# Performance work log

Measured on AMD Instinct MI355X. Metric: run time of the kernel, lower is better.

Reference implementation:

```python
import jax, jax.numpy as jnp
import numpy as np

H = 2048        # hidden_size
NH = 16         # num query heads
NKV = 4         # num kv heads
HD = H // NH    # head_dim = 128
G = NH // NKV   # kv groups = 4
EPS = 1e-12


def setup_inputs() -> dict:
    key = jax.random.key(0)
    ks = jax.random.split(key, 20)
    B, S = 2, 2048
    s = 1.0 / np.sqrt(H)
    inp = {
        "hidden_states": jax.random.normal(ks[0], (B, S, H), jnp.float32),
        "source_states": jax.random.normal(ks[1], (B, S, H), jnp.float32),
        # weights stored [in, out] so y = x @ W + b
        "Wq": jax.random.normal(ks[2], (H, NH * HD), jnp.float32) * s,
        "bq": jnp.zeros((NH * HD,), jnp.float32),
        "Wk": jax.random.normal(ks[3], (H, NKV * HD), jnp.float32) * s,
        "bk": jnp.zeros((NKV * HD,), jnp.float32),
        "Wv": jax.random.normal(ks[4], (H, NKV * HD), jnp.float32) * s,
        "bv": jnp.zeros((NKV * HD,), jnp.float32),
        "Wd": jax.random.normal(ks[5], (H, H), jnp.float32) * s,
        "bd": jnp.zeros((H,), jnp.float32),
        "W1": jax.random.normal(ks[6], (H, H), jnp.float32) * s,
        "b1": jnp.zeros((H,), jnp.float32),
        "W2": jax.random.normal(ks[7], (H, H), jnp.float32) * s,
        "b2": jnp.zeros((H,), jnp.float32),
        "gamma": jnp.ones((H,), jnp.float32),
        "beta": jnp.zeros((H,), jnp.float32),
    }
    return inp


def _layernorm(x, gamma, beta):
    mu = jnp.mean(x, axis=-1, keepdims=True)
    var = jnp.mean(jnp.square(x - mu), axis=-1, keepdims=True)
    return (x - mu) * jax.lax.rsqrt(var + EPS) * gamma + beta


def reference(hidden_states, source_states, Wq, bq, Wk, bk, Wv, bv, Wd, bd,
              W1, b1, W2, b2, gamma, beta):
    B, Sq, _ = hidden_states.shape
    Ss = source_states.shape[1]
    # FFN-gate on source: Pl1 = relu(lin1(src)); P = lin2(Pl1) + Pl1
    Pl1 = jax.nn.relu(source_states @ W1 + b1)
    P = (Pl1 @ W2 + b2) + Pl1
    # projections; K/V grouped into NKV heads, Q into NH = NKV*G heads
    K = (P @ Wk + bk).reshape(B, Ss, NKV, HD).transpose(0, 2, 1, 3)        # b k s d
    V = (P @ Wv + bv).reshape(B, Ss, NKV, HD).transpose(0, 2, 1, 3)        # b k s d
    Q = (hidden_states @ Wq + bq).reshape(B, Sq, NKV, G, HD)
    Q = Q.transpose(0, 2, 3, 1, 4)                                          # b k g q d
    scores = jnp.einsum('bkgqd,bksd->bkgqs', Q, K) / np.sqrt(HD)
    probs = jax.nn.softmax(scores, axis=-1)
    ctx = jnp.einsum('bkgqs,bksd->bkgqd', probs, V)                         # b k g q d
    ctx = ctx.transpose(0, 3, 1, 2, 4).reshape(B, Sq, NH * HD)              # b q h*d
    out = ctx @ Wd + bd
    return _layernorm(out + hidden_states, gamma, beta)
```

## Files before the change

kernel.cpp:

```cpp
#include <hip/hip_runtime.h>
#include <hip/hip_bf16.h>

typedef __bf16 bf16;
typedef __bf16 bf16x4 __attribute__((ext_vector_type(4)));
typedef __bf16 bf16x8 __attribute__((ext_vector_type(8)));
typedef float  f32x4  __attribute__((ext_vector_type(4)));

#define H_   2048
#define S_   2048
#define B_   2
#define NH_  16
#define NKV_ 4
#define HD_  128
#define KVS  1024

#define QSCALE 0.12751743f

__device__ __forceinline__ f32x4 mfma16(bf16x8 a, bf16x8 b, f32x4 c) {
  return __builtin_amdgcn_mfma_f32_16x16x32_bf16(a, b, c, 0, 0, 0);
}

typedef __attribute__((address_space(3))) unsigned int lds_u32_t;
typedef const __attribute__((address_space(1))) unsigned int glb_u32_t;
__device__ __forceinline__ void glds16(const bf16* g, bf16* l) {
  __builtin_amdgcn_global_load_lds((glb_u32_t*)g, (lds_u32_t*)l, 16, 0, 0);
}

__global__ __launch_bounds__(256)
void prep(const float* __restrict__ Wq, const float* __restrict__ W1,
          const float* __restrict__ W2, const float* __restrict__ Wd,
          const float* __restrict__ Wk, const float* __restrict__ Wv,
          const float* __restrict__ hidden, const float* __restrict__ source,
          bf16* __restrict__ Wqt, bf16* __restrict__ W1t,
          bf16* __restrict__ W2t, bf16* __restrict__ Wdt,
          bf16* __restrict__ Wkt, bf16* __restrict__ Wvt,
          bf16* __restrict__ hb,  bf16* __restrict__ sb)
{
  __shared__ bf16 t[32][33];
  int idx = blockIdx.x;
  if (idx < 16384) {
    const float* in = (idx < 8192) ? hidden : source;
    bf16*       out = (idx < 8192) ? hb : sb;
    const int i = idx & 8191;
    const size_t off = ((size_t)i * 256 + threadIdx.x) * 4;
    const float4 v = *(const float4*)(in + off);
    bf16x4 o = { (bf16)v.x, (bf16)v.y, (bf16)v.z, (bf16)v.w };
    *(bf16x4*)(out + off) = o;
    return;
  }
  idx -= 16384;
  const float* in; bf16* out; int N;
  if      (idx < 4096)  { in = Wq; out = Wqt; N = 2048; }
  else if (idx < 8192)  { in = W1; out = W1t; N = 2048; idx -= 4096; }
  else if (idx < 12288) { in = W2; out = W2t; N = 2048; idx -= 8192; }
  else if (idx < 16384) { in = Wd; out = Wdt; N = 2048; idx -= 12288; }
  else if (idx < 17408) { in = Wk; out = Wkt; N = 512;  idx -= 16384; }
  else                  { in = Wv; out = Wvt; N = 512;  idx -= 17408; }
  const int K = 2048;
  const int tx = threadIdx.x & 31, ty = threadIdx.x >> 5;
  const int k0 = (idx & 63) * 32, n0 = (idx >> 6) * 32;
  #pragma unroll
  for (int i = 0; i < 4; i++)
    t[ty + i*8][tx] = (bf16)in[(size_t)(k0 + ty + i*8) * N + n0 + tx];
  __syncthreads();
  #pragma unroll
  for (int i = 0; i < 4; i++)
    out[(size_t)(n0 + ty + i*8) * K + k0 + tx] = t[tx][ty + i*8];
}

__global__ __launch_bounds__(256)
void transpose_v(const bf16* __restrict__ KVin, bf16* __restrict__ Vt)
{
  __shared__ bf16 t[32][33];
  const int tx = threadIdx.x & 31, ty = threadIdx.x >> 5;
  const int s0 = blockIdx.x * 32, d0 = blockIdx.y * 32;
  const int bk = blockIdx.z;
  const int b = bk >> 2, kv = bk & 3;
  const bf16* src = KVin + (size_t)b * S_ * KVS + 512 + kv * HD_;
  #pragma unroll
  for (int i = 0; i < 4; i++)
    t[ty + i*8][tx] = src[(size_t)(s0 + ty + i*8) * KVS + d0 + tx];
  __syncthreads();
  bf16* dst = Vt + (size_t)bk * HD_ * S_;
  #pragma unroll
  for (int i = 0; i < 4; i++)
    dst[(size_t)(d0 + ty + i*8) * S_ + s0 + tx] = t[tx][ty + i*8];
}

__device__ __forceinline__
void gemm_body(const bf16* __restrict__ A, const bf16* __restrict__ Wt,
               const float* __restrict__ bias, const float* __restrict__ bias2,
               int nsplit, const bf16* __restrict__ resid,
               bf16* __restrict__ outB, int N, int K, int relu, float oscale,
               int m0, int n0, bf16* As, bf16* Bs)
{
  const int tid  = threadIdx.x;
  const int lane = tid & 63;
  const int w    = tid >> 6;
  const int wm = w & 1, wn = w >> 1;
  const int quad = lane >> 4, l16 = lane & 15;
  const int g_r = lane >> 2;
  const int g_c = (lane & 3) * 8;

  const f32x4 fz = {0.f, 0.f, 0.f, 0.f};
  f32x4 acc[4][4];
  #pragma unroll
  for (int i = 0; i < 4; i++)
    #pragma unroll
    for (int j = 0; j < 4; j++) acc[i][j] = fz;

  auto stage = [&](int nb, int k0) {
    #pragma unroll
    for (int i = 0; i < 2; i++) {
      const int rb = (w*2 + i) * 16;
      glds16(A  + (size_t)(m0 + rb + g_r) * K + k0 + g_c, As + nb*4096 + rb*32 + lane*8);
      glds16(Wt + (size_t)(n0 + rb + g_r) * K + k0 + g_c, Bs + nb*4096 + rb*32 + lane*8);
    }
  };

  stage(0, 0);
  const int NK = K >> 5;
  for (int it = 0; it < NK; it++) {
    const int bf = it & 1;
    __syncthreads();
    if (it + 1 < NK) stage(bf ^ 1, (it + 1) << 5);
    bf16x8 af[4], bfr[4];
    #pragma unroll
    for (int i = 0; i < 4; i++)
      af[i]  = *(const bf16x8*)(As + bf*4096 + (wm*64 + i*16 + l16)*32 + quad*8);
    #pragma unroll
    for (int j = 0; j < 4; j++)
      bfr[j] = *(const bf16x8*)(Bs + bf*4096 + (wn*64 + j*16 + l16)*32 + quad*8);
    #pragma unroll
    for (int i = 0; i < 4; i++)
      #pragma unroll
      for (int j = 0; j < 4; j++)
        acc[i][j] = mfma16(af[i], bfr[j], acc[i][j]);
  }

  #pragma unroll
  for (int i = 0; i < 4; i++) {
    const int row = m0 + wm*64 + i*16 + quad*4;
    #pragma unroll
    for (int j = 0; j < 4; j++) {
      const int col = n0 + wn*64 + j*16 + l16;
      const float bi = (col < nsplit) ? bias[col] : bias2[col - nsplit];
      #pragma unroll
      for (int r = 0; r < 4; r++) {
        float v = acc[i][j][r] + bi;
        if (relu) v = fmaxf(v, 0.f);
        v *= oscale;
        size_t idx = (size_t)(row + r) * N + col;
        if (resid) v += (float)resid[idx];
        outB[idx] = (bf16)v;
      }
    }
  }
}

__global__ __launch_bounds__(256)
void gemm_one(const bf16* __restrict__ A, const bf16* __restrict__ Wt,
              const float* __restrict__ bias, const float* __restrict__ bias2,
              int nsplit, const bf16* __restrict__ resid,
              bf16* __restrict__ outB, int N, int K, int relu, float oscale)
{
  __shared__ __align__(16) bf16 As[2*128*32];
  __shared__ __align__(16) bf16 Bs[2*128*32];
  gemm_body(A, Wt, bias, bias2, nsplit, resid, outB, N, K, relu, oscale,
            blockIdx.y*128, blockIdx.x*128, As, Bs);
}

__global__ __launch_bounds__(256)
void gemm_dual(const bf16* __restrict__ A0, const bf16* __restrict__ W0,
               const float* __restrict__ b0, bf16* __restrict__ o0,
               int relu0, float s0,
               const bf16* __restrict__ A1, const bf16* __restrict__ W1,
               const float* __restrict__ b1, bf16* __restrict__ o1,
               int relu1, float s1, int N, int K)
{
  __shared__ __align__(16) bf16 As[2*128*32];
  __shared__ __align__(16) bf16 Bs[2*128*32];
  if (blockIdx.z == 0)
    gemm_body(A0, W0, b0, b0, 1<<30, nullptr, o0, N, K, relu0, s0,
              blockIdx.y*128, blockIdx.x*128, As, Bs);
  else
    gemm_body(A1, W1, b1, b1, 1<<30, nullptr, o1, N, K, relu1, s1,
              blockIdx.y*128, blockIdx.x*128, As, Bs);
}

__global__ __launch_bounds__(256)
void attn_partial(const bf16* __restrict__ Q, const bf16* __restrict__ KV,
                  const bf16* __restrict__ Vt, bf16* __restrict__ OpBase,
                  float* __restrict__ LsBase)
{
  __shared__ __align__(16) bf16 Ks[2][4][32][32];
  __shared__ __align__(16) bf16 Vs[2][8][16][32];
  __shared__ __align__(16) bf16 Ps[4][32][40];
  const int tid = threadIdx.x;
  const int lane = tid & 63, w = tid >> 6;
  const int quad = lane >> 4, l16 = lane & 15;
  const int qt = blockIdx.x, h = blockIdx.y;
  const int b = blockIdx.z >> 1, sh = blockIdx.z & 1;
  const int kv = h >> 2;
  const int qbase = qt * 128 + w * 32;
  const int s_begin = sh * (S_/2);

  bf16*  Op = OpBase + (size_t)sh * 8388608;
  float* Lp = LsBase + (size_t)sh * (B_*NH_*S_);

  const bf16* Qp = Q  + ((size_t)b * S_ + qbase) * H_ + h * HD_;
  const bf16* Kp = KV + (size_t)b * S_ * KVS + kv * HD_;
  const bf16* Vp = Vt + (size_t)(b * NKV_ + kv) * HD_ * S_;

  const int g_r = lane >> 2;
  const int g_c = (lane & 3) * 8;

  const f32x4 fz = {0.f, 0.f, 0.f, 0.f};

  bf16x8 qf[2][4];
  #pragma unroll
  for (int i = 0; i < 2; i++)
    #pragma unroll
    for (int kt = 0; kt < 4; kt++)
      qf[i][kt] = *(const bf16x8*)(Qp + (size_t)(i*16 + l16) * H_ + kt*32 + quad*8);

  f32x4 o[2][8];
  #pragma unroll
  for (int i = 0; i < 2; i++)
    #pragma unroll
    for (int n = 0; n < 8; n++) o[i][n] = fz;
  float lsum[2][4];
  #pragma unroll
  for (int i = 0; i < 2; i++)
    #pragma unroll
    for (int r = 0; r < 4; r++) lsum[i][r] = 0.f;

  const int rd_sw = ((l16 >> 2) & 3) * 8;

  {
    const int s0 = s_begin;
    glds16(Kp + (size_t)(s0 +      g_r) * KVS + w*32 + g_c, &Ks[0][w][0][0]   + lane*8);
    glds16(Kp + (size_t)(s0 + 16 + g_r) * KVS + w*32 + g_c, &Ks[0][w][16][0]  + lane*8);
    glds16(Vp + (size_t)(w*16     + g_r) * S_ + s0 + g_c,   &Vs[0][w][0][0]   + lane*8);
    glds16(Vp + (size_t)((4+w)*16 + g_r) * S_ + s0 + g_c,   &Vs[0][4+w][0][0] + lane*8);
  }

  const int NIT = (S_/2) / 32;
  for (int it = 0; it < NIT; it++) {
    const int bf = it & 1;
    __syncthreads();
    if (it + 1 < NIT) {
      const int s0 = s_begin + (it + 1) * 32;
      const int nb = bf ^ 1;
      glds16(Kp + (size_t)(s0 +      g_r) * KVS + w*32 + g_c, &Ks[nb][w][0][0]   + lane*8);
      glds16(Kp + (size_t)(s0 + 16 + g_r) * KVS + w*32 + g_c, &Ks[nb][w][16][0]  + lane*8);
      glds16(Vp + (size_t)(w*16     + g_r) * S_ + s0 + g_c,   &Vs[nb][w][0][0]   + lane*8);
      glds16(Vp + (size_t)((4+w)*16 + g_r) * S_ + s0 + g_c,   &Vs[nb][4+w][0][0] + lane*8);
    }

    f32x4 sa[2][2];
    sa[0][0] = fz; sa[0][1] = fz; sa[1][0] = fz; sa[1][1] = fz;
    #pragma unroll
    for (int kt = 0; kt < 4; kt++) {
      bf16x8 kf0 = *(const bf16x8*)(&Ks[bf][kt][l16][quad*8]);
      bf16x8 kf1 = *(const bf16x8*)(&Ks[bf][kt][16 + l16][quad*8]);
      #pragma unroll
      for (int i = 0; i < 2; i++) {
        sa[i][0] = mfma16(qf[i][kt], kf0, sa[i][0]);
        sa[i][1] = mfma16(qf[i][kt], kf1, sa[i][1]);
      }
    }
    #pragma unroll
    for (int i = 0; i < 2; i++)
      #pragma unroll
      for (int nt = 0; nt < 2; nt++)
        #pragma unroll
        for (int r = 0; r < 4; r++) {
          float p = exp2f(sa[i][nt][r]);
          lsum[i][r] += p;
          Ps[w][i*16 + quad*4 + r][(nt*16 + l16) ^ (quad*8)] = (bf16)p;
        }
    bf16x8 pf[2];
    #pragma unroll
    for (int i = 0; i < 2; i++)
      pf[i] = *(const bf16x8*)(&Ps[w][i*16 + l16][(quad*8) ^ rd_sw]);
    #pragma unroll
    for (int nt = 0; nt < 8; nt++) {
      bf16x8 vf = *(const bf16x8*)(&Vs[bf][nt][l16][quad*8]);
      #pragma unroll
      for (int i = 0; i < 2; i++)
        o[i][nt] = mfma16(pf[i], vf, o[i][nt]);
    }
  }

  #pragma unroll
  for (int i = 0; i < 2; i++)
    #pragma unroll
    for (int r = 0; r < 4; r++) {
      float s = lsum[i][r];
      s += __shfl_xor(s, 1);
      s += __shfl_xor(s, 2);
      s += __shfl_xor(s, 4);
      s += __shfl_xor(s, 8);
      lsum[i][r] = s;
    }

  bf16* op = Op + ((size_t)b * S_ + qbase) * H_ + h * HD_;
  #pragma unroll
  for (int i = 0; i < 2; i++)
    #pragma unroll
    for (int nt = 0; nt < 8; nt++)
      #pragma unroll
      for (int r = 0; r < 4; r++)
        op[(size_t)(i*16 + quad*4 + r) * H_ + nt*16 + l16] = (bf16)o[i][nt][r];
  if (l16 == 0) {
    float* lp = Lp + (size_t)(b * NH_ + h) * S_ + qbase;
    #pragma unroll
    for (int i = 0; i < 2; i++)
      #pragma unroll
      for (int r = 0; r < 4; r++)
        lp[i*16 + quad*4 + r] = lsum[i][r];
  }
}

__global__ __launch_bounds__(256)
void attn_combine(const bf16* __restrict__ O0, const bf16* __restrict__ O1,
                  const float* __restrict__ L0, const float* __restrict__ L1,
                  bf16* __restrict__ ctx)
{
  const int row = blockIdx.x;
  const int b = row >> 11, s = row & 2047;
  const int tid = threadIdx.x;
  const int h = tid >> 4;
  const size_t idx = (size_t)row * H_ + tid * 8;
  const size_t li  = (size_t)(b * NH_ + h) * S_ + s;
  const float rinv = 1.f / (L0[li] + L1[li]);
  bf16x8 a = *(const bf16x8*)(O0 + idx);
  bf16x8 c = *(const bf16x8*)(O1 + idx);
  bf16x8 o;
  #pragma unroll
  for (int k = 0; k < 8; k++)
    o[k] = (bf16)(((float)a[k] + (float)c[k]) * rinv);
  *(bf16x8*)(ctx + idx) = o;
}

__global__ __launch_bounds__(256)
void ln_fused(const bf16* __restrict__ a, const float* __restrict__ hidden,
              const float* __restrict__ gamma, const float* __restrict__ beta,
              float* __restrict__ out)
{
  __shared__ float red[8];
  const int row = blockIdx.x;
  const bf16*  pa = a      + (size_t)row * H_;
  const float* pb = hidden + (size_t)row * H_;
  float x[8]; float s = 0.f, s2 = 0.f;
  #pragma unroll
  for (int j = 0; j < 8; j++) {
    int c = threadIdx.x + j*256;
    float v = (float)pa[c] + pb[c];
    x[j] = v; s += v; s2 += v*v;
  }
  #pragma unroll
  for (int off = 1; off < 64; off <<= 1) {
    s  += __shfl_xor(s,  off);
    s2 += __shfl_xor(s2, off);
  }
  const int wv = threadIdx.x >> 6;
  if ((threadIdx.x & 63) == 0) { red[wv] = s; red[4 + wv] = s2; }
  __syncthreads();
  s  = red[0] + red[1] + red[2] + red[3];
  s2 = red[4] + red[5] + red[6] + red[7];
  const float mu   = s * (1.0f / H_);
  const float var  = s2 * (1.0f / H_) - mu * mu;
  const float rstd = rsqrtf(var + 1e-12f);
  float* po = out + (size_t)row * H_;
  #pragma unroll
  for (int j = 0; j < 8; j++) {
    int c = threadIdx.x + j*256;
    po[c] = ((x[j] - mu) * rstd) * gamma[c] + beta[c];
  }
}

extern "C" void kernel_launch(void* const* d_in, const int* in_sizes, int n_in,
                              void* d_out, int out_size, void* d_ws, size_t ws_size,
                              hipStream_t stream)
{
  (void)in_sizes; (void)n_in; (void)out_size; (void)ws_size;
  const float* hidden = (const float*)d_in[0];
  const float* source = (const float*)d_in[1];
  const float* Wq = (const float*)d_in[2];
  const float* bq = (const float*)d_in[3];
  const float* Wk = (const float*)d_in[4];
  const float* bk = (const float*)d_in[5];
  const float* Wv = (const float*)d_in[6];
  const float* bv = (const float*)d_in[7];
  const float* Wd = (const float*)d_in[8];
  const float* bd = (const float*)d_in[9];
  const float* W1 = (const float*)d_in[10];
  const float* b1 = (const float*)d_in[11];
  const float* W2 = (const float*)d_in[12];
  const float* b2 = (const float*)d_in[13];
  const float* gamma = (const float*)d_in[14];
  const float* beta  = (const float*)d_in[15];

  char* ws = (char*)d_ws;
  const size_t M = 1048576;
  bf16*  rHB = (bf16*)(ws + 0*M);
  bf16*  rSB = (bf16*)(ws + 16*M);
  bf16*  Qb  = (bf16*)(ws + 32*M);
  bf16*  Wqt = (bf16*)(ws + 48*M);
  bf16*  W2t = (bf16*)(ws + 56*M);
  bf16*  W1t = (bf16*)(ws + 64*M);
  bf16*  Wdt = (bf16*)(ws + 72*M);
  bf16*  Wkt = (bf16*)(ws + 80*M);
  bf16*  Wvt = (bf16*)(ws + 82*M);
  bf16*  Pl1 = (bf16*)(ws + 84*M);
  bf16*  KVb = (bf16*)(ws + 84*M);
  bf16*  Vtb = (bf16*)(ws + 92*M);
  float* Ls  = (float*)(ws + 48*M);
  bf16*  Pb  = rHB;
  bf16*  O0  = rHB;
  bf16*  O1  = rSB;
  bf16*  ctx = (bf16*)(ws + 56*M);
  bf16*  oFb = Qb;

  prep<<<34816, 256, 0, stream>>>(Wq, W1, W2, Wd, Wk, Wv, hidden, source,
                                  Wqt, W1t, W2t, Wdt, Wkt, Wvt, rHB, rSB);
  gemm_dual<<<dim3(16,32,2), 256, 0, stream>>>(
      rHB, Wqt, bq, Qb,  0, QSCALE,
      rSB, W1t, b1, Pl1, 1, 1.0f, 2048, 2048);
  gemm_one<<<dim3(16,32), 256, 0, stream>>>(Pl1, W2t, b2, b2, 1<<30, Pl1,
                                            Pb, 2048, 2048, 0, 1.0f);
  gemm_one<<<dim3(8,32), 256, 0, stream>>>(Pb, Wkt, bk, bv, 512, nullptr,
                                           KVb, 1024, 2048, 0, 1.0f);
  transpose_v<<<dim3(64,4,8), 256, 0, stream>>>(KVb, Vtb);
  attn_partial<<<dim3(16,16,4), 256, 0, stream>>>(Qb, KVb, Vtb, O0, Ls);
  attn_combine<<<4096, 256, 0, stream>>>(O0, O1, Ls, Ls + B_*NH_*S_, ctx);
  gemm_one<<<dim3(16,32), 256, 0, stream>>>(ctx, Wdt, bd, bd, 1<<30, nullptr,
                                            oFb, 2048, 2048, 0, 1.0f);
  ln_fused<<<4096, 256, 0, stream>>>(oFb, hidden, gamma, beta, (float*)d_out);
}
```

Before: 600.9 us.

## Keep attention probabilities in registers via transposed QK MFMA and lane shuffles

The QK^T MFMA operands are swapped so each lane holds scores for one query row. The probabilities are then packed to bf16 and redistributed with lane shuffles into the PV A-operand layout, replacing the LDS round trip through the Ps buffer. K/V staging now uses a flat fragment-major LDS layout so fragment reads are contiguous per lane. The change also adds s_setprio around the MFMA blocks and launch_bounds(256,4) to raise occupancy, at the cost of extra shuffle instructions and register pressure.

```diff
diff --git a/kernel.cpp b/kernel.cpp
--- a/kernel.cpp
+++ b/kernel.cpp
@@ -2,9 +2,11 @@
 #include <hip/hip_bf16.h>
 
 typedef __bf16 bf16;
+typedef __bf16 bf16x2 __attribute__((ext_vector_type(2)));
 typedef __bf16 bf16x4 __attribute__((ext_vector_type(4)));
 typedef __bf16 bf16x8 __attribute__((ext_vector_type(8)));
 typedef float  f32x4  __attribute__((ext_vector_type(4)));
+typedef unsigned int u32x4 __attribute__((ext_vector_type(4)));
 
 #define H_   2048
 #define S_   2048
@@ -24,6 +26,11 @@
 typedef const __attribute__((address_space(1))) unsigned int glb_u32_t;
 __device__ __forceinline__ void glds16(const bf16* g, bf16* l) {
   __builtin_amdgcn_global_load_lds((glb_u32_t*)g, (lds_u32_t*)l, 16, 0, 0);
+}
+
+__device__ __forceinline__ unsigned pk2(float a, float b) {
+  bf16x2 v = { (bf16)a, (bf16)b };
+  return __builtin_bit_cast(unsigned, v);
 }
 
 __global__ __launch_bounds__(256)
@@ -188,14 +195,13 @@
               blockIdx.y*128, blockIdx.x*128, As, Bs);
 }
 
-__global__ __launch_bounds__(256)
+__global__ __launch_bounds__(256, 4)
 void attn_partial(const bf16* __restrict__ Q, const bf16* __restrict__ KV,
                   const bf16* __restrict__ Vt, bf16* __restrict__ OpBase,
                   float* __restrict__ LsBase)
 {
-  __shared__ __align__(16) bf16 Ks[2][4][32][32];
-  __shared__ __align__(16) bf16 Vs[2][8][16][32];
-  __shared__ __align__(16) bf16 Ps[4][32][40];
+  __shared__ __align__(16) bf16 Ks[2*4096];
+  __shared__ __align__(16) bf16 Vs[2*4096];
   const int tid = threadIdx.x;
   const int lane = tid & 63, w = tid >> 6;
   const int quad = lane >> 4, l16 = lane & 15;
@@ -212,8 +218,8 @@
   const bf16* Kp = KV + (size_t)b * S_ * KVS + kv * HD_;
   const bf16* Vp = Vt + (size_t)(b * NKV_ + kv) * HD_ * S_;
 
-  const int g_r = lane >> 2;
-  const int g_c = (lane & 3) * 8;
+  const int fr = lane & 15;
+  const int fc = (lane >> 4) * 8;
 
   const f32x4 fz = {0.f, 0.f, 0.f, 0.f};
 
@@ -229,81 +235,80 @@
   for (int i = 0; i < 2; i++)
     #pragma unroll
     for (int n = 0; n < 8; n++) o[i][n] = fz;
-  float lsum[2][4];
-  #pragma unroll
-  for (int i = 0; i < 2; i++)
-    #pragma unroll
-    for (int r = 0; r < 4; r++) lsum[i][r] = 0.f;
-
-  const int rd_sw = ((l16 >> 2) & 3) * 8;
-
-  {
-    const int s0 = s_begin;
-    glds16(Kp + (size_t)(s0 +      g_r) * KVS + w*32 + g_c, &Ks[0][w][0][0]   + lane*8);
-    glds16(Kp + (size_t)(s0 + 16 + g_r) * KVS + w*32 + g_c, &Ks[0][w][16][0]  + lane*8);
-    glds16(Vp + (size_t)(w*16     + g_r) * S_ + s0 + g_c,   &Vs[0][w][0][0]   + lane*8);
-    glds16(Vp + (size_t)((4+w)*16 + g_r) * S_ + s0 + g_c,   &Vs[0][4+w][0][0] + lane*8);
-  }
+  float lsum[2] = {0.f, 0.f};
+
+  auto stageKV = [&](int nb, int s0) {
+    bf16* Kb = Ks + nb*4096;
+    bf16* Vb = Vs + nb*4096;
+    glds16(Kp + (size_t)(s0 +      fr) * KVS + w*32 + fc, Kb + (w*2+0)*512 + lane*8);
+    glds16(Kp + (size_t)(s0 + 16 + fr) * KVS + w*32 + fc, Kb + (w*2+1)*512 + lane*8);
+    glds16(Vp + (size_t)(w*16     + fr) * S_ + s0 + fc,   Vb + w*512       + lane*8);
+    glds16(Vp + (size_t)((4+w)*16 + fr) * S_ + s0 + fc,   Vb + (4+w)*512   + lane*8);
+  };
+
+  stageKV(0, s_begin);
 
   const int NIT = (S_/2) / 32;
   for (int it = 0; it < NIT; it++) {
     const int bf = it & 1;
     __syncthreads();
-    if (it + 1 < NIT) {
-      const int s0 = s_begin + (it + 1) * 32;
-      const int nb = bf ^ 1;
-      glds16(Kp + (size_t)(s0 +      g_r) * KVS + w*32 + g_c, &Ks[nb][w][0][0]   + lane*8);
-      glds16(Kp + (size_t)(s0 + 16 + g_r) * KVS + w*32 + g_c, &Ks[nb][w][16][0]  + lane*8);
-      glds16(Vp + (size_t)(w*16     + g_r) * S_ + s0 + g_c,   &Vs[nb][w][0][0]   + lane*8);
-      glds16(Vp + (size_t)((4+w)*16 + g_r) * S_ + s0 + g_c,   &Vs[nb][4+w][0][0] + lane*8);
-    }
-
+    if (it + 1 < NIT) stageKV(bf ^ 1, s_begin + (it + 1) * 32);
+
+    const bf16* Kb = Ks + bf*4096;
     f32x4 sa[2][2];
     sa[0][0] = fz; sa[0][1] = fz; sa[1][0] = fz; sa[1][1] = fz;
+    __builtin_amdgcn_s_setprio(1);
     #pragma unroll
     for (int kt = 0; kt < 4; kt++) {
-      bf16x8 kf0 = *(const bf16x8*)(&Ks[bf][kt][l16][quad*8]);
-      bf16x8 kf1 = *(const bf16x8*)(&Ks[bf][kt][16 + l16][quad*8]);
+      bf16x8 kf0 = *(const bf16x8*)(Kb + (kt*2+0)*512 + lane*8);
+      bf16x8 kf1 = *(const bf16x8*)(Kb + (kt*2+1)*512 + lane*8);
       #pragma unroll
       for (int i = 0; i < 2; i++) {
-        sa[i][0] = mfma16(qf[i][kt], kf0, sa[i][0]);
-        sa[i][1] = mfma16(qf[i][kt], kf1, sa[i][1]);
+        sa[i][0] = mfma16(kf0, qf[i][kt], sa[i][0]);
+        sa[i][1] = mfma16(kf1, qf[i][kt], sa[i][1]);
       }
     }
-    #pragma unroll
-    for (int i = 0; i < 2; i++)
+    __builtin_amdgcn_s_setprio(0);
+
+    bf16x8 pf[2];
+    #pragma unroll
+    for (int i = 0; i < 2; i++) {
+      float p[2][4];
       #pragma unroll
       for (int nt = 0; nt < 2; nt++)
         #pragma unroll
         for (int r = 0; r < 4; r++) {
-          float p = exp2f(sa[i][nt][r]);
-          lsum[i][r] += p;
-          Ps[w][i*16 + quad*4 + r][(nt*16 + l16) ^ (quad*8)] = (bf16)p;
+          p[nt][r] = exp2f(sa[i][nt][r]);
+          lsum[i] += p[nt][r];
         }
-    bf16x8 pf[2];
-    #pragma unroll
-    for (int i = 0; i < 2; i++)
-      pf[i] = *(const bf16x8*)(&Ps[w][i*16 + l16][(quad*8) ^ rd_sw]);
+      unsigned Apk = pk2(p[0][0], p[0][1]);
+      unsigned Bpk = pk2(p[0][2], p[0][3]);
+      unsigned Cpk = pk2(p[1][0], p[1][1]);
+      unsigned Dpk = pk2(p[1][2], p[1][3]);
+      const int srcL = l16 + ((quad & 1) << 5);
+      const bool hi = (quad >= 2);
+      const unsigned a0 = __shfl(Apk, srcL),      b0 = __shfl(Bpk, srcL);
+      const unsigned a1 = __shfl(Apk, srcL + 16), b1 = __shfl(Bpk, srcL + 16);
+      const unsigned c0 = __shfl(Cpk, srcL),      d0 = __shfl(Dpk, srcL);
+      const unsigned c1 = __shfl(Cpk, srcL + 16), d1 = __shfl(Dpk, srcL + 16);
+      u32x4 t;
+      t.x = hi ? c0 : a0;
+      t.y = hi ? d0 : b0;
+      t.z = hi ? c1 : a1;
+      t.w = hi ? d1 : b1;
+      pf[i] = __builtin_bit_cast(bf16x8, t);
+    }
+
+    const bf16* Vb = Vs + bf*4096;
+    __builtin_amdgcn_s_setprio(1);
     #pragma unroll
     for (int nt = 0; nt < 8; nt++) {
-      bf16x8 vf = *(const bf16x8*)(&Vs[bf][nt][l16][quad*8]);
-      #pragma unroll
-      for (int i = 0; i < 2; i++)
-        o[i][nt] = mfma16(pf[i], vf, o[i][nt]);
+      bf16x8 vf = *(const bf16x8*)(Vb + nt*512 + lane*8);
+      o[0][nt] = mfma16(pf[0], vf, o[0][nt]);
+      o[1][nt] = mfma16(pf[1], vf, o[1][nt]);
     }
-  }
-
-  #pragma unroll
-  for (int i = 0; i < 2; i++)
-    #pragma unroll
-    for (int r = 0; r < 4; r++) {
-      float s = lsum[i][r];
-      s += __shfl_xor(s, 1);
-      s += __shfl_xor(s, 2);
-      s += __shfl_xor(s, 4);
-      s += __shfl_xor(s, 8);
-      lsum[i][r] = s;
-    }
+    __builtin_amdgcn_s_setprio(0);
+  }
 
   bf16* op = Op + ((size_t)b * S_ + qbase) * H_ + h * HD_;
   #pragma unroll
@@ -313,13 +318,14 @@
       #pragma unroll
       for (int r = 0; r < 4; r++)
         op[(size_t)(i*16 + quad*4 + r) * H_ + nt*16 + l16] = (bf16)o[i][nt][r];
-  if (l16 == 0) {
-    float* lp = Lp + (size_t)(b * NH_ + h) * S_ + qbase;
-    #pragma unroll
-    for (int i = 0; i < 2; i++)
-      #pragma unroll
-      for (int r = 0; r < 4; r++)
-        lp[i*16 + quad*4 + r] = lsum[i][r];
+
+  float* lp = Lp + (size_t)(b * NH_ + h) * S_ + qbase;
+  #pragma unroll
+  for (int i = 0; i < 2; i++) {
+    float s = lsum[i];
+    s += __shfl_xor(s, 16);
+    s += __shfl_xor(s, 32);
+    if (lane < 16) lp[i*16 + lane] = s;
   }
 }
 
```

Measured after the change: 642.4 us. +6.9%, slower.
